# Kernel tuning notes

Measured on AMD Instinct MI355X. Metric: run time of the kernel, lower is better.

## Reference

```python
import jax, jax.numpy as jnp
import numpy as np

N = 100000      # nodes
E = 1600000     # edges
NSG2 = 20000    # subgraph2 count
NSG = 2000      # subgraph count
NG = 64         # graphs
D = 64          # hidden dim
L = 5           # conv layers


def setup_inputs() -> dict:
    key = jax.random.key(0)
    ks = jax.random.split(key, 40)
    f = lambda i, shape: (jax.random.normal(ks[i], shape, jnp.float32) * 0.05)
    inp = {
        'z': jax.random.randint(ks[0], (N, 2), 0, 100),
        'edge_index': jax.random.randint(ks[1], (2, E), 0, N),
        'node_to_subgraph2': jax.random.randint(ks[2], (N,), 0, NSG2),
        'subgraph2_to_subgraph': jax.random.randint(ks[3], (NSG2,), 0, NSG),
        'subgraph_to_graph': jax.random.randint(ks[4], (NSG,), 0, NG),
        # learned params (stacked across the 5 layers where identical shape)
        'z_emb': f(5, (L, 100, D)),
        'trans_W': f(6, (L - 1, 2 * D, D)),  # transform_before_conv, layers 1..4
        'trans_b': f(7, (L - 1, D)),
        'conv_W': f(8, (L, D, D)),           # GatedGraphConv weight (num_layers=1)
        'gru_Wih': f(9, (L, D, 3 * D)),
        'gru_bih': f(10, (L, 3 * D)),
        'gru_Whh': f(11, (L, D, 3 * D)),
        'gru_bhh': f(12, (L, 3 * D)),
        'ep_W1': f(13, (D, D)), 'ep_b1': f(14, (D,)),
        'ep_W2': f(15, (D, D)), 'ep_b2': f(16, (D,)),
        'np_W1': f(17, (D, D)), 'np_b1': f(18, (D,)),
        'np_W2': f(19, (D, D)), 'np_b2': f(20, (D,)),
        'fc1_W': f(21, (D, 32)), 'fc1_b': f(22, (32,)),
        'fc2_W': f(23, (32, 16)), 'fc2_b': f(24, (16,)),
        'fc3_W': f(25, (16, 1)), 'fc3_b': f(26, (1,)),
    }
    return inp


def _gated_conv(x, src, dst, W, Wih, bih, Whh, bhh):
    # GatedGraphConv(out=64, num_layers=1): m = aggr_add(x_j @ W), x = GRUCell(m, x)
    h = x @ W                                            # [N, D]
    m = jax.ops.segment_sum(h[src], dst, num_segments=N)  # scatter-add messages
    gi = m @ Wih + bih                                   # [N, 3D]
    gh = x @ Whh + bhh
    ir, iz, inn = jnp.split(gi, 3, axis=-1)
    hr, hz, hn = jnp.split(gh, 3, axis=-1)
    r = jax.nn.sigmoid(ir + hr)
    zg = jax.nn.sigmoid(iz + hz)
    n = jnp.tanh(inn + r * hn)
    return (1.0 - zg) * n + zg * x


def reference(z, edge_index, node_to_subgraph2, subgraph2_to_subgraph, subgraph_to_graph,
              z_emb, trans_W, trans_b, conv_W, gru_Wih, gru_bih, gru_Whh, gru_bhh,
              ep_W1, ep_b1, ep_W2, ep_b2, np_W1, np_b1, np_W2, np_b2,
              fc1_W, fc1_b, fc2_W, fc2_b, fc3_W, fc3_b):
    src, dst = edge_index[0], edge_index[1]
    x = None
    for layer in range(L):
        ze = z_emb[layer][z].sum(axis=1)  # [N,2,D] -> [N,D]
        if x is None:
            x = ze
        else:
            x = jnp.concatenate([x, ze], axis=-1) @ trans_W[layer - 1] + trans_b[layer - 1]
        x = _gated_conv(x, src, dst, conv_W[layer], gru_Wih[layer], gru_bih[layer],
                        gru_Whh[layer], gru_bhh[layer])
    # 3-level add pooling with MLPs in between
    x = jax.ops.segment_sum(x, node_to_subgraph2, num_segments=NSG2)
    x = jax.nn.relu(x @ ep_W1 + ep_b1) @ ep_W2 + ep_b2
    x = jax.ops.segment_sum(x, subgraph2_to_subgraph, num_segments=NSG)
    x = jax.nn.relu(x @ np_W1 + np_b1) @ np_W2 + np_b2
    x = jax.ops.segment_sum(x, subgraph_to_graph, num_segments=NG)
    x = jax.nn.elu(x @ fc1_W + fc1_b)
    x = jax.nn.elu(x @ fc2_W + fc2_b)
    return x @ fc3_W + fc3_b  # [NG, 1]
```

## Files before the change

### kernel.cpp

```cpp
#include <hip/hip_runtime.h>
#include <hip/hip_bf16.h>

constexpr int N    = 100000;
constexpr int E    = 1600000;
constexpr int NSG2 = 20000;
constexpr int NSG  = 2000;
constexpr int NG   = 64;
constexpr int D    = 64;
constexpr int L    = 5;

constexpr int NPB   = 32;
constexpr int NBUCK = N / NPB;
constexpr int NSTR  = 8;
constexpr int SCAP  = 128;

typedef __attribute__((ext_vector_type(8))) short short8v;
typedef __attribute__((ext_vector_type(4))) float f32x4;

__device__ __forceinline__ float sigm(float x) { return 1.0f / (1.0f + expf(-x)); }
__device__ __forceinline__ float elu(float x)  { return x > 0.0f ? x : (expf(x) - 1.0f); }

__device__ __forceinline__ unsigned short f2b(float f) {
    union { float f; unsigned u; } x; x.f = f;
    unsigned r = (x.u + 0x7FFFu + ((x.u >> 16) & 1u)) >> 16;
    return (unsigned short)r;
}
__device__ __forceinline__ float b2f(unsigned short h) {
    union { unsigned u; float f; } x; x.u = (unsigned)h << 16;
    return x.f;
}

__global__ __launch_bounds__(256) void prep_kernel(const float* __restrict__ convW,
                                                   const float* __restrict__ Wih,
                                                   float* __restrict__ WihP) {
    int idx = blockIdx.x * 256 + threadIdx.x;
    if (idx >= L * 64 * 192) return;
    int l = idx / (64 * 192);
    int rem = idx % (64 * 192);
    int i = rem / 192, j = rem % 192;
    const float* W  = convW + l * 64 * 64;
    const float* Wi = Wih  + l * 64 * 192;
    float acc = 0.0f;
    for (int t = 0; t < 64; ++t) acc = fmaf(W[i * 64 + t], Wi[t * 192 + j], acc);
    WihP[idx] = acc;
}

__global__ __launch_bounds__(256) void packg_kernel(const float* __restrict__ WihP,
                                                    const float* __restrict__ gWhh,
                                                    unsigned short* __restrict__ Wgpk) {
    int idx = blockIdx.x * 256 + threadIdx.x;
    if (idx >= L * 2 * 12 * 2 * 64) return;
    int lane = idx & 63;
    int r1 = idx >> 6;
    int t  = r1 & 1;
    int r2 = r1 >> 1;
    int nt = r2 % 12;
    int lm = r2 / 12;
    int mat = lm & 1, l = lm >> 1;
    const float* W = mat ? (gWhh + (size_t)l * 64 * 192) : (WihP + (size_t)l * 64 * 192);
    int n  = nt * 16 + (lane & 15);
    int k0 = t * 32 + (lane >> 4) * 8;
    short8v v;
#pragma unroll
    for (int j = 0; j < 8; ++j) v[j] = (short)f2b(W[(k0 + j) * 192 + n]);
    *(short8v*)(Wgpk + (size_t)idx * 8) = v;
}

__global__ __launch_bounds__(256) void packt_kernel(const float* __restrict__ tW,
                                                    unsigned short* __restrict__ tWpk) {
    int idx = blockIdx.x * 256 + threadIdx.x;
    if (idx >= (L - 1) * 4 * 4 * 64) return;
    int lane = idx & 63;
    int r1 = idx >> 6;
    int t  = r1 & 3;
    int r2 = r1 >> 2;
    int nt = r2 & 3;
    int lm = r2 >> 2;
    const float* W = tW + (size_t)lm * 128 * 64;
    int n  = nt * 16 + (lane & 15);
    int k0 = t * 32 + (lane >> 4) * 8;
    short8v v;
#pragma unroll
    for (int j = 0; j < 8; ++j) v[j] = (short)f2b(W[(k0 + j) * 64 + n]);
    *(short8v*)(tWpk + (size_t)idx * 8) = v;
}

__global__ void bucketA_kernel(const int* __restrict__ src, const int* __restrict__ dst,
                               int* __restrict__ bcnt, unsigned* __restrict__ tmp) {
    int stripe = blockIdx.x & (NSTR - 1);
    for (int e = blockIdx.x * blockDim.x + threadIdx.x; e < E; e += gridDim.x * blockDim.x) {
        int d = dst[e];
        int cell = (d >> 5) * NSTR + stripe;
        int pos = atomicAdd(&bcnt[cell * 16], 1);
        if (pos < SCAP)
            tmp[(size_t)cell * SCAP + pos] = ((unsigned)(d & 31) << 17) | (unsigned)src[e];
    }
}

__global__ __launch_bounds__(1024) void bscan_kernel(const int* __restrict__ bcnt,
                                                     int* __restrict__ bbase,
                                                     int* __restrict__ rowptrN) {
    __shared__ int part[1024];
    int t = threadIdx.x;
    int loc[4]; int sum = 0;
#pragma unroll
    for (int j = 0; j < 4; ++j) {
        int b = t * 4 + j; int v = 0;
        if (b < NBUCK) {
#pragma unroll
            for (int s = 0; s < NSTR; ++s) v += min(bcnt[(b * NSTR + s) * 16], SCAP);
        }
        loc[j] = v; sum += v;
    }
    part[t] = sum;
    __syncthreads();
    for (int off = 1; off < 1024; off <<= 1) {
        int u = (t >= off) ? part[t - off] : 0;
        __syncthreads();
        part[t] += u;
        __syncthreads();
    }
    int run = part[t] - sum;
#pragma unroll
    for (int j = 0; j < 4; ++j) {
        int b = t * 4 + j;
        if (b < NBUCK) bbase[b] = run;
        run += loc[j];
    }
    if (t == 1023) { bbase[NBUCK] = part[1023]; rowptrN[0] = part[1023]; }
}

__global__ __launch_bounds__(256) void bucketB_kernel(const unsigned* __restrict__ tmp,
                                                      const int* __restrict__ bcnt,
                                                      const int* __restrict__ bbase,
                                                      int* __restrict__ rowptr,
                                                      int* __restrict__ col) {
    __shared__ unsigned recs[NSTR * SCAP];
    __shared__ int scnt[NSTR];
    __shared__ int soff[NSTR + 1];
    __shared__ int cur[NPB];
    int b = blockIdx.x, tid = threadIdx.x;
    if (tid < NSTR) scnt[tid] = min(bcnt[(b * NSTR + tid) * 16], SCAP);
    if (tid < NPB) cur[tid] = 0;
    __syncthreads();
    if (tid == 0) {
        int r = 0;
        for (int s = 0; s < NSTR; ++s) { soff[s] = r; r += scnt[s]; }
        soff[NSTR] = r;
    }
    __syncthreads();
    int total = soff[NSTR];
    for (int i = tid; i < NSTR * SCAP; i += 256) {
        int s = i >> 7, k = i & (SCAP - 1);
        if (k < scnt[s]) recs[soff[s] + k] = tmp[((size_t)b * NSTR + s) * SCAP + k];
    }
    __syncthreads();
    for (int i = tid; i < total; i += 256) atomicAdd(&cur[recs[i] >> 17], 1);
    __syncthreads();
    if (tid == 0) {
        int base = bbase[b], r = 0;
        for (int j = 0; j < NPB; ++j) {
            int v = cur[j];
            cur[j] = base + r;
            rowptr[b * NPB + j] = base + r;
            r += v;
        }
    }
    __syncthreads();
    for (int i = tid; i < total; i += 256) {
        unsigned w = recs[i];
        int pos = atomicAdd(&cur[w >> 17], 1);
        col[pos] = (int)(w & 0x1FFFFu);
    }
}

__global__ __launch_bounds__(256) void embed_kernel(const int* __restrict__ z,
                                                    const float* __restrict__ zemb0,
                                                    float* __restrict__ x,
                                                    unsigned short* __restrict__ xb) {
    int idx = blockIdx.x * 256 + threadIdx.x;
    if (idx >= N * D) return;
    int n = idx >> 6, c = idx & 63;
    float v = zemb0[z[n * 2] * 64 + c] + zemb0[z[n * 2 + 1] * 64 + c];
    x[idx] = v;
    xb[idx] = f2b(v);
}

__global__ __launch_bounds__(256) void aggregate_kernel(const unsigned short* __restrict__ xb,
                                                        const int* __restrict__ rowptr,
                                                        const int* __restrict__ col,
                                                        unsigned short* __restrict__ sb) {
    int node = blockIdx.x * 4 + (threadIdx.x >> 6);
    int lane = threadIdx.x & 63;
    if (node >= N) return;
    int grp = lane >> 3;
    int cl  = lane & 7;
    int beg = rowptr[node], end = rowptr[node + 1];

    float a[8] = {};
    int i = beg + grp;
    for (; i + 8 < end; i += 16) {
        int u0 = col[i], u1 = col[i + 8];
        short8v v0 = *(const short8v*)(xb + (size_t)u0 * 64 + cl * 8);
        short8v v1 = *(const short8v*)(xb + (size_t)u1 * 64 + cl * 8);
#pragma unroll
        for (int j = 0; j < 8; ++j)
            a[j] += b2f((unsigned short)v0[j]) + b2f((unsigned short)v1[j]);
    }
    if (i < end) {
        int u = col[i];
        short8v v = *(const short8v*)(xb + (size_t)u * 64 + cl * 8);
#pragma unroll
        for (int j = 0; j < 8; ++j) a[j] += b2f((unsigned short)v[j]);
    }
#pragma unroll
    for (int off = 8; off < 64; off <<= 1)
#pragma unroll
        for (int j = 0; j < 8; ++j) a[j] += __shfl_xor(a[j], off, 64);
    if (grp == 0) {
        short8v r;
#pragma unroll
        for (int j = 0; j < 8; ++j) r[j] = (short)f2b(a[j]);
        *(short8v*)(sb + (size_t)node * 64 + cl * 8) = r;
    }
}

__global__ __launch_bounds__(256) void gru_mfma_kernel(const unsigned short* __restrict__ sb,
                                                       float* __restrict__ xbuf,
                                                       unsigned short* __restrict__ xb,
                                                       const unsigned short* __restrict__ Wgpk_l,
                                                       const float* __restrict__ bih,
                                                       const float* __restrict__ bhh) {
    __shared__ unsigned short s_lds[32][72];
    __shared__ unsigned short x_lds[32][72];
    int tid = threadIdx.x;
    int node0 = blockIdx.x * 32;

    {
        const float4* sb4 = (const float4*)(sb + (size_t)node0 * 64);
        const float4* xb4 = (const float4*)(xb + (size_t)node0 * 64);
        int r = tid >> 3, u = tid & 7;
        *(float4*)&s_lds[r][u * 8] = sb4[tid];
        *(float4*)&x_lds[r][u * 8] = xb4[tid];
    }
    __syncthreads();

    int lane = tid & 63, w = tid >> 6;
    int lr = lane & 15, lg = lane >> 4;

    short8v as_[2][2], ax_[2][2];
#pragma unroll
    for (int mt = 0; mt < 2; ++mt)
#pragma unroll
        for (int t = 0; t < 2; ++t) {
            int row = mt * 16 + lr, koff = t * 32 + lg * 8;
            as_[mt][t] = *(const short8v*)&s_lds[row][koff];
            ax_[mt][t] = *(const short8v*)&x_lds[row][koff];
        }

    f32x4 accA[3][2] = {};
    f32x4 accB[3][2] = {};
#pragma unroll
    for (int g = 0; g < 3; ++g) {
        int nt = g * 4 + w;
#pragma unroll
        for (int t = 0; t < 2; ++t) {
            const unsigned short* pA = Wgpk_l + ((size_t)((0 * 12 + nt) * 2 + t) * 64 + lane) * 8;
            const unsigned short* pB = Wgpk_l + ((size_t)((1 * 12 + nt) * 2 + t) * 64 + lane) * 8;
            short8v bA = *(const short8v*)pA;
            short8v bB = *(const short8v*)pB;
#pragma unroll
            for (int mt = 0; mt < 2; ++mt) {
                accA[g][mt] = __builtin_amdgcn_mfma_f32_16x16x32_bf16(as_[mt][t], bA, accA[g][mt], 0, 0, 0);
                accB[g][mt] = __builtin_amdgcn_mfma_f32_16x16x32_bf16(ax_[mt][t], bB, accB[g][mt], 0, 0, 0);
            }
        }
    }

    int ch = w * 16 + lr;
    float bi0 = bih[ch], bi1 = bih[64 + ch], bi2 = bih[128 + ch];
    float bh0 = bhh[ch], bh1 = bhh[64 + ch], bh2 = bhh[128 + ch];
#pragma unroll
    for (int mt = 0; mt < 2; ++mt) {
#pragma unroll
        for (int reg = 0; reg < 4; ++reg) {
            int m = mt * 16 + lg * 4 + reg;
            float r  = sigm(accA[0][mt][reg] + bi0 + accB[0][mt][reg] + bh0);
            float zg = sigm(accA[1][mt][reg] + bi1 + accB[1][mt][reg] + bh1);
            float nn = tanhf(accA[2][mt][reg] + bi2 + r * (accB[2][mt][reg] + bh2));
            size_t o = (size_t)(node0 + m) * 64 + ch;
            float xo = (1.0f - zg) * nn + zg * xbuf[o];
            xbuf[o] = xo;
            xb[o] = f2b(xo);
        }
    }
}

__global__ __launch_bounds__(256) void trans_mfma_kernel(const int* __restrict__ z,
                                                         const float* __restrict__ zemb_l,
                                                         const unsigned short* __restrict__ tWpk_l,
                                                         const float* __restrict__ tb,
                                                         float* __restrict__ xbuf,
                                                         unsigned short* __restrict__ xb) {
    __shared__ unsigned short a_lds[32][136];
    int tid = threadIdx.x;
    int node0 = blockIdx.x * 32;

    {
        const float4* xb4 = (const float4*)(xb + (size_t)node0 * 64);
        int r = tid >> 3, u = tid & 7;
        *(float4*)&a_lds[r][u * 8] = xb4[tid];
    }
#pragma unroll
    for (int it = 0; it < 8; ++it) {
        int idx = it * 256 + tid;
        int n = idx >> 6, k = idx & 63;
        int z0 = z[(node0 + n) * 2], z1 = z[(node0 + n) * 2 + 1];
        float ze = zemb_l[z0 * 64 + k] + zemb_l[z1 * 64 + k];
        a_lds[n][64 + k] = f2b(ze);
    }
    __syncthreads();

    int lane = tid & 63, w = tid >> 6;
    int lr = lane & 15, lg = lane >> 4;

    f32x4 acc[2] = {};
#pragma unroll
    for (int t = 0; t < 4; ++t) {
        const unsigned short* pB = tWpk_l + ((size_t)(w * 4 + t) * 64 + lane) * 8;
        short8v bf = *(const short8v*)pB;
#pragma unroll
        for (int mt = 0; mt < 2; ++mt) {
            int row = mt * 16 + lr, koff = t * 32 + lg * 8;
            short8v af = *(const short8v*)&a_lds[row][koff];
            acc[mt] = __builtin_amdgcn_mfma_f32_16x16x32_bf16(af, bf, acc[mt], 0, 0, 0);
        }
    }
    int ch = w * 16 + lr;
    float tbc = tb[ch];
#pragma unroll
    for (int mt = 0; mt < 2; ++mt)
#pragma unroll
        for (int reg = 0; reg < 4; ++reg) {
            int m = mt * 16 + lg * 4 + reg;
            size_t o = (size_t)(node0 + m) * 64 + ch;
            float v = acc[mt][reg] + tbc;
            xbuf[o] = v;
            xb[o] = f2b(v);
        }
}

__global__ void pool_kernel(const float* __restrict__ in, const int* __restrict__ idx,
                            float* __restrict__ out, int rows) {
    int i = blockIdx.x * 256 + threadIdx.x;
    if (i >= rows * 64) return;
    int r = i >> 6, c = i & 63;
    atomicAdd(out + (size_t)idx[r] * 64 + c, in[i]);
}

__global__ __launch_bounds__(256) void mlp_kernel(float* __restrict__ buf,
                                                  const float* __restrict__ W1,
                                                  const float* __restrict__ b1,
                                                  const float* __restrict__ W2,
                                                  const float* __restrict__ b2) {
    __shared__ float in_t[4][64];
    __shared__ float h_t[4][64];
    int tid = threadIdx.x;
    int c = tid & 63, r = tid >> 6;
    int row0 = blockIdx.x * 4;
    in_t[r][c] = buf[(size_t)(row0 + r) * 64 + c];
    __syncthreads();
    float acc = b1[c];
    for (int k = 0; k < 64; ++k) acc = fmaf(in_t[r][k], W1[k * 64 + c], acc);
    h_t[r][c] = fmaxf(acc, 0.0f);
    __syncthreads();
    acc = b2[c];
    for (int k = 0; k < 64; ++k) acc = fmaf(h_t[r][k], W2[k * 64 + c], acc);
    buf[(size_t)(row0 + r) * 64 + c] = acc;
}

__global__ __launch_bounds__(256) void final_kernel(const float* __restrict__ g,
                                                    const float* __restrict__ fc1W, const float* __restrict__ fc1b,
                                                    const float* __restrict__ fc2W, const float* __restrict__ fc2b,
                                                    const float* __restrict__ fc3W, const float* __restrict__ fc3b,
                                                    float* __restrict__ out) {
    __shared__ float gt[64][64];
    __shared__ float h1[64][32];
    __shared__ float h2[64][16];
    int tid = threadIdx.x;
    for (int i = tid; i < 64 * 64; i += 256) gt[i >> 6][i & 63] = g[i];
    __syncthreads();
    for (int i = tid; i < 64 * 32; i += 256) {
        int r = i >> 5, c = i & 31;
        float acc = fc1b[c];
        for (int k = 0; k < 64; ++k) acc = fmaf(gt[r][k], fc1W[k * 32 + c], acc);
        h1[r][c] = elu(acc);
    }
    __syncthreads();
    for (int i = tid; i < 64 * 16; i += 256) {
        int r = i >> 4, c = i & 15;
        float acc = fc2b[c];
        for (int k = 0; k < 32; ++k) acc = fmaf(h1[r][k], fc2W[k * 16 + c], acc);
        h2[r][c] = elu(acc);
    }
    __syncthreads();
    if (tid < 64) {
        float acc = fc3b[0];
        for (int k = 0; k < 16; ++k) acc = fmaf(h2[tid][k], fc3W[k], acc);
        out[tid] = acc;
    }
}

extern "C" void kernel_launch(void* const* d_in, const int* in_sizes, int n_in,
                              void* d_out, int out_size, void* d_ws, size_t ws_size,
                              hipStream_t stream) {
    const int*   z     = (const int*)d_in[0];
    const int*   ei    = (const int*)d_in[1];
    const int*   n2s2  = (const int*)d_in[2];
    const int*   s22s  = (const int*)d_in[3];
    const int*   s2g   = (const int*)d_in[4];
    const float* z_emb = (const float*)d_in[5];
    const float* tW    = (const float*)d_in[6];
    const float* tb    = (const float*)d_in[7];
    const float* convW = (const float*)d_in[8];
    const float* gWih  = (const float*)d_in[9];
    const float* gbih  = (const float*)d_in[10];
    const float* gWhh  = (const float*)d_in[11];
    const float* gbhh  = (const float*)d_in[12];
    const float* epW1  = (const float*)d_in[13];
    const float* epb1  = (const float*)d_in[14];
    const float* epW2  = (const float*)d_in[15];
    const float* epb2  = (const float*)d_in[16];
    const float* npW1  = (const float*)d_in[17];
    const float* npb1  = (const float*)d_in[18];
    const float* npW2  = (const float*)d_in[19];
    const float* npb2  = (const float*)d_in[20];
    const float* fc1W  = (const float*)d_in[21];
    const float* fc1b  = (const float*)d_in[22];
    const float* fc2W  = (const float*)d_in[23];
    const float* fc2b  = (const float*)d_in[24];
    const float* fc3W  = (const float*)d_in[25];
    const float* fc3b  = (const float*)d_in[26];

    const int* srcp = ei;
    const int* dstp = ei + E;

    float*          xbuf = (float*)d_ws;
    unsigned short* xb   = (unsigned short*)(xbuf + (size_t)N * D);
    unsigned short* sb   = xb + (size_t)N * D;
    float*          WihP = (float*)(sb + (size_t)N * D);
    int*            rowptr = (int*)(WihP + L * 64 * 192);
    int*            colbuf = rowptr + (N + 1);
    int*            bbase  = colbuf + E;
    uintptr_t pal = (uintptr_t)(bbase + NBUCK + 1);
    pal = (pal + 15) & ~(uintptr_t)15;
    unsigned short* Wgpk = (unsigned short*)pal;
    unsigned short* tWpk = Wgpk + (size_t)L * 2 * 12 * 2 * 64 * 8;
    unsigned* tmp  = (unsigned*)xbuf;
    int*      bcnt = (int*)(tmp + (size_t)NBUCK * NSTR * SCAP);
    float* sg2  = (float*)colbuf;
    float* sg   = sg2 + (size_t)NSG2 * D;
    float* gbuf = sg + (size_t)NSG * D;

    hipMemsetAsync(bcnt, 0, (size_t)NBUCK * NSTR * 16 * sizeof(int), stream);

    prep_kernel<<<(L * 64 * 192 + 255) / 256, 256, 0, stream>>>(convW, gWih, WihP);
    packg_kernel<<<(L * 2 * 12 * 2 * 64 + 255) / 256, 256, 0, stream>>>(WihP, gWhh, Wgpk);
    packt_kernel<<<((L - 1) * 4 * 4 * 64 + 255) / 256, 256, 0, stream>>>(tW, tWpk);

    bucketA_kernel<<<4096, 256, 0, stream>>>(srcp, dstp, bcnt, tmp);
    bscan_kernel<<<1, 1024, 0, stream>>>(bcnt, bbase, rowptr + N);
    bucketB_kernel<<<NBUCK, 256, 0, stream>>>(tmp, bcnt, bbase, rowptr, colbuf);

    embed_kernel<<<(N * D + 255) / 256, 256, 0, stream>>>(z, z_emb, xbuf, xb);

    for (int l = 0; l < L; ++l) {
        if (l > 0) {
            trans_mfma_kernel<<<N / 32, 256, 0, stream>>>(
                z, z_emb + (size_t)l * 100 * 64,
                tWpk + (size_t)(l - 1) * 4 * 4 * 64 * 8,
                tb + (size_t)(l - 1) * 64, xbuf, xb);
        }
        aggregate_kernel<<<(N + 3) / 4, 256, 0, stream>>>(xb, rowptr, colbuf, sb);
        gru_mfma_kernel<<<N / 32, 256, 0, stream>>>(
            sb, xbuf, xb,
            Wgpk + (size_t)l * 2 * 12 * 2 * 64 * 8,
            gbih + (size_t)l * 192, gbhh + (size_t)l * 192);
    }

    hipMemsetAsync(sg2, 0, (size_t)(NSG2 + NSG + NG) * D * sizeof(float), stream);
    pool_kernel<<<(N * D + 255) / 256, 256, 0, stream>>>(xbuf, n2s2, sg2, N);
    mlp_kernel<<<NSG2 / 4, 256, 0, stream>>>(sg2, epW1, epb1, epW2, epb2);
    pool_kernel<<<(NSG2 * D + 255) / 256, 256, 0, stream>>>(sg2, s22s, sg, NSG2);
    mlp_kernel<<<NSG / 4, 256, 0, stream>>>(sg, npW1, npb1, npW2, npb2);
    pool_kernel<<<(NSG * D + 255) / 256, 256, 0, stream>>>(sg, s2g, gbuf, NSG);
    final_kernel<<<1, 256, 0, stream>>>(gbuf, fc1W, fc1b, fc2W, fc2b, fc3W, fc3b, (float*)d_out);
}
```

Baseline: 570.7 us.

## Fuse aggregation, GRU update and next-layer transform into one per-layer kernel

Merges the CSR neighbor aggregation, the GRU MFMA update and the following layer's transform into a single kernel per layer. Bf16 node features are ping-ponged between two buffers so that one layer's gather reads do not race with its writes. This removes the sb round trip through global memory, the intermediate xbuf/xb writes and two launches per layer. The cost is that aggregation is now done by one 8-lane group per node with a serial edge loop, which gives less memory-level parallelism than the previous 64-lane-per-node gather, and it raises LDS use per block. The embed kernel is also vectorized to float4.

```diff
diff --git a/kernel.cpp b/kernel.cpp
--- a/kernel.cpp
+++ b/kernel.cpp
@@ -179,75 +179,66 @@
                                                     float* __restrict__ x,
                                                     unsigned short* __restrict__ xb) {
     int idx = blockIdx.x * 256 + threadIdx.x;
-    if (idx >= N * D) return;
-    int n = idx >> 6, c = idx & 63;
-    float v = zemb0[z[n * 2] * 64 + c] + zemb0[z[n * 2 + 1] * 64 + c];
-    x[idx] = v;
-    xb[idx] = f2b(v);
-}
-
-__global__ __launch_bounds__(256) void aggregate_kernel(const unsigned short* __restrict__ xb,
-                                                        const int* __restrict__ rowptr,
-                                                        const int* __restrict__ col,
-                                                        unsigned short* __restrict__ sb) {
-    int node = blockIdx.x * 4 + (threadIdx.x >> 6);
-    int lane = threadIdx.x & 63;
-    if (node >= N) return;
-    int grp = lane >> 3;
-    int cl  = lane & 7;
-    int beg = rowptr[node], end = rowptr[node + 1];
-
-    float a[8] = {};
-    int i = beg + grp;
-    for (; i + 8 < end; i += 16) {
-        int u0 = col[i], u1 = col[i + 8];
-        short8v v0 = *(const short8v*)(xb + (size_t)u0 * 64 + cl * 8);
-        short8v v1 = *(const short8v*)(xb + (size_t)u1 * 64 + cl * 8);
-#pragma unroll
-        for (int j = 0; j < 8; ++j)
-            a[j] += b2f((unsigned short)v0[j]) + b2f((unsigned short)v1[j]);
-    }
-    if (i < end) {
-        int u = col[i];
-        short8v v = *(const short8v*)(xb + (size_t)u * 64 + cl * 8);
-#pragma unroll
-        for (int j = 0; j < 8; ++j) a[j] += b2f((unsigned short)v[j]);
-    }
-#pragma unroll
-    for (int off = 8; off < 64; off <<= 1)
-#pragma unroll
-        for (int j = 0; j < 8; ++j) a[j] += __shfl_xor(a[j], off, 64);
-    if (grp == 0) {
-        short8v r;
-#pragma unroll
-        for (int j = 0; j < 8; ++j) r[j] = (short)f2b(a[j]);
-        *(short8v*)(sb + (size_t)node * 64 + cl * 8) = r;
-    }
-}
-
-__global__ __launch_bounds__(256) void gru_mfma_kernel(const unsigned short* __restrict__ sb,
-                                                       float* __restrict__ xbuf,
-                                                       unsigned short* __restrict__ xb,
-                                                       const unsigned short* __restrict__ Wgpk_l,
-                                                       const float* __restrict__ bih,
-                                                       const float* __restrict__ bhh) {
+    if (idx >= N * 16) return;
+    int n = idx >> 4, k4 = idx & 15;
+    float4 e0 = ((const float4*)(zemb0 + (size_t)z[n * 2] * 64))[k4];
+    float4 e1 = ((const float4*)(zemb0 + (size_t)z[n * 2 + 1] * 64))[k4];
+    float4 v; v.x = e0.x + e1.x; v.y = e0.y + e1.y; v.z = e0.z + e1.z; v.w = e0.w + e1.w;
+    ((float4*)x)[idx] = v;
+    ushort4 b; b.x = f2b(v.x); b.y = f2b(v.y); b.z = f2b(v.z); b.w = f2b(v.w);
+    ((ushort4*)xb)[idx] = b;
+}
+
+template<int HAS_T>
+__global__ __launch_bounds__(256) void fused_kernel(const unsigned short* __restrict__ xb_in,
+                                                    float* __restrict__ xbuf,
+                                                    unsigned short* __restrict__ xb_out,
+                                                    const int* __restrict__ rowptr,
+                                                    const int* __restrict__ col,
+                                                    const unsigned short* __restrict__ Wgpk_l,
+                                                    const float* __restrict__ bih,
+                                                    const float* __restrict__ bhh,
+                                                    const int* __restrict__ z,
+                                                    const float* __restrict__ zemb_next,
+                                                    const unsigned short* __restrict__ tWpk_next,
+                                                    const float* __restrict__ tb_next) {
     __shared__ unsigned short s_lds[32][72];
     __shared__ unsigned short x_lds[32][72];
+    __shared__ unsigned short a_lds[32][136];
     int tid = threadIdx.x;
     int node0 = blockIdx.x * 32;
+    int lane = tid & 63, w = tid >> 6;
 
     {
-        const float4* sb4 = (const float4*)(sb + (size_t)node0 * 64);
-        const float4* xb4 = (const float4*)(xb + (size_t)node0 * 64);
-        int r = tid >> 3, u = tid & 7;
-        *(float4*)&s_lds[r][u * 8] = sb4[tid];
-        *(float4*)&x_lds[r][u * 8] = xb4[tid];
-    }
-    __syncthreads();
-
-    int lane = tid & 63, w = tid >> 6;
+        int g8 = lane >> 3, cj = lane & 7;
+        int nl = w * 8 + g8;
+        int node = node0 + nl;
+        int beg = rowptr[node], end = rowptr[node + 1];
+        float a[8] = {};
+        int i = beg;
+        for (; i + 1 < end; i += 2) {
+            int u0 = col[i], u1 = col[i + 1];
+            short8v v0 = *(const short8v*)(xb_in + (size_t)u0 * 64 + cj * 8);
+            short8v v1 = *(const short8v*)(xb_in + (size_t)u1 * 64 + cj * 8);
+#pragma unroll
+            for (int j = 0; j < 8; ++j)
+                a[j] += b2f((unsigned short)v0[j]) + b2f((unsigned short)v1[j]);
+        }
+        if (i < end) {
+            int u = col[i];
+            short8v v = *(const short8v*)(xb_in + (size_t)u * 64 + cj * 8);
+#pragma unroll
+            for (int j = 0; j < 8; ++j) a[j] += b2f((unsigned short)v[j]);
+        }
+        short8v r;
+#pragma unroll
+        for (int j = 0; j < 8; ++j) r[j] = (short)f2b(a[j]);
+        *(short8v*)&s_lds[nl][cj * 8] = r;
+        *(float4*)&x_lds[nl][cj * 8] = ((const float4*)(xb_in + (size_t)node * 64))[cj];
+    }
+    __syncthreads();
+
     int lr = lane & 15, lg = lane >> 4;
-
     short8v as_[2][2], ax_[2][2];
 #pragma unroll
     for (int mt = 0; mt < 2; ++mt)
@@ -280,6 +271,7 @@
     int ch = w * 16 + lr;
     float bi0 = bih[ch], bi1 = bih[64 + ch], bi2 = bih[128 + ch];
     float bh0 = bhh[ch], bh1 = bhh[64 + ch], bh2 = bhh[128 + ch];
+    float xo[2][4];
 #pragma unroll
     for (int mt = 0; mt < 2; ++mt) {
 #pragma unroll
@@ -288,65 +280,64 @@
             float r  = sigm(accA[0][mt][reg] + bi0 + accB[0][mt][reg] + bh0);
             float zg = sigm(accA[1][mt][reg] + bi1 + accB[1][mt][reg] + bh1);
             float nn = tanhf(accA[2][mt][reg] + bi2 + r * (accB[2][mt][reg] + bh2));
-            size_t o = (size_t)(node0 + m) * 64 + ch;
-            float xo = (1.0f - zg) * nn + zg * xbuf[o];
-            xbuf[o] = xo;
-            xb[o] = f2b(xo);
-        }
-    }
-}
-
-__global__ __launch_bounds__(256) void trans_mfma_kernel(const int* __restrict__ z,
-                                                         const float* __restrict__ zemb_l,
-                                                         const unsigned short* __restrict__ tWpk_l,
-                                                         const float* __restrict__ tb,
-                                                         float* __restrict__ xbuf,
-                                                         unsigned short* __restrict__ xb) {
-    __shared__ unsigned short a_lds[32][136];
-    int tid = threadIdx.x;
-    int node0 = blockIdx.x * 32;
-
-    {
-        const float4* xb4 = (const float4*)(xb + (size_t)node0 * 64);
-        int r = tid >> 3, u = tid & 7;
-        *(float4*)&a_lds[r][u * 8] = xb4[tid];
-    }
-#pragma unroll
-    for (int it = 0; it < 8; ++it) {
+            xo[mt][reg] = (1.0f - zg) * nn + zg * xbuf[(size_t)(node0 + m) * 64 + ch];
+        }
+    }
+
+    if (HAS_T == 0) {
+#pragma unroll
+        for (int mt = 0; mt < 2; ++mt)
+#pragma unroll
+            for (int reg = 0; reg < 4; ++reg) {
+                int m = mt * 16 + lg * 4 + reg;
+                xbuf[(size_t)(node0 + m) * 64 + ch] = xo[mt][reg];
+            }
+        return;
+    }
+
+#pragma unroll
+    for (int mt = 0; mt < 2; ++mt)
+#pragma unroll
+        for (int reg = 0; reg < 4; ++reg) {
+            int m = mt * 16 + lg * 4 + reg;
+            a_lds[m][ch] = f2b(xo[mt][reg]);
+        }
+#pragma unroll
+    for (int it = 0; it < 2; ++it) {
         int idx = it * 256 + tid;
-        int n = idx >> 6, k = idx & 63;
+        int n = idx >> 4, k4 = idx & 15;
         int z0 = z[(node0 + n) * 2], z1 = z[(node0 + n) * 2 + 1];
-        float ze = zemb_l[z0 * 64 + k] + zemb_l[z1 * 64 + k];
-        a_lds[n][64 + k] = f2b(ze);
-    }
-    __syncthreads();
-
-    int lane = tid & 63, w = tid >> 6;
-    int lr = lane & 15, lg = lane >> 4;
-
-    f32x4 acc[2] = {};
+        float4 e0 = ((const float4*)(zemb_next + (size_t)z0 * 64))[k4];
+        float4 e1 = ((const float4*)(zemb_next + (size_t)z1 * 64))[k4];
+        ushort4 b;
+        b.x = f2b(e0.x + e1.x); b.y = f2b(e0.y + e1.y);
+        b.z = f2b(e0.z + e1.z); b.w = f2b(e0.w + e1.w);
+        *(ushort4*)&a_lds[n][64 + k4 * 4] = b;
+    }
+    __syncthreads();
+
+    f32x4 tacc[2] = {};
 #pragma unroll
     for (int t = 0; t < 4; ++t) {
-        const unsigned short* pB = tWpk_l + ((size_t)(w * 4 + t) * 64 + lane) * 8;
+        const unsigned short* pB = tWpk_next + ((size_t)(w * 4 + t) * 64 + lane) * 8;
         short8v bf = *(const short8v*)pB;
 #pragma unroll
         for (int mt = 0; mt < 2; ++mt) {
             int row = mt * 16 + lr, koff = t * 32 + lg * 8;
             short8v af = *(const short8v*)&a_lds[row][koff];
-            acc[mt] = __builtin_amdgcn_mfma_f32_16x16x32_bf16(af, bf, acc[mt], 0, 0, 0);
-        }
-    }
-    int ch = w * 16 + lr;
-    float tbc = tb[ch];
+            tacc[mt] = __builtin_amdgcn_mfma_f32_16x16x32_bf16(af, bf, tacc[mt], 0, 0, 0);
+        }
+    }
+    float tbc = tb_next[ch];
 #pragma unroll
     for (int mt = 0; mt < 2; ++mt)
 #pragma unroll
         for (int reg = 0; reg < 4; ++reg) {
             int m = mt * 16 + lg * 4 + reg;
             size_t o = (size_t)(node0 + m) * 64 + ch;
-            float v = acc[mt][reg] + tbc;
+            float v = tacc[mt][reg] + tbc;
             xbuf[o] = v;
-            xb[o] = f2b(v);
+            xb_out[o] = f2b(v);
         }
 }
 
@@ -446,9 +437,9 @@
     const int* dstp = ei + E;
 
     float*          xbuf = (float*)d_ws;
-    unsigned short* xb   = (unsigned short*)(xbuf + (size_t)N * D);
-    unsigned short* sb   = xb + (size_t)N * D;
-    float*          WihP = (float*)(sb + (size_t)N * D);
+    unsigned short* xbA  = (unsigned short*)(xbuf + (size_t)N * D);
+    unsigned short* xbB  = xbA + (size_t)N * D;
+    float*          WihP = (float*)(xbB + (size_t)N * D);
     int*            rowptr = (int*)(WihP + L * 64 * 192);
     int*            colbuf = rowptr + (N + 1);
     int*            bbase  = colbuf + E;
@@ -472,20 +463,25 @@
     bscan_kernel<<<1, 1024, 0, stream>>>(bcnt, bbase, rowptr + N);
     bucketB_kernel<<<NBUCK, 256, 0, stream>>>(tmp, bcnt, bbase, rowptr, colbuf);
 
-    embed_kernel<<<(N * D + 255) / 256, 256, 0, stream>>>(z, z_emb, xbuf, xb);
+    embed_kernel<<<(N * 16 + 255) / 256, 256, 0, stream>>>(z, z_emb, xbuf, xbA);
 
     for (int l = 0; l < L; ++l) {
-        if (l > 0) {
-            trans_mfma_kernel<<<N / 32, 256, 0, stream>>>(
-                z, z_emb + (size_t)l * 100 * 64,
-                tWpk + (size_t)(l - 1) * 4 * 4 * 64 * 8,
-                tb + (size_t)(l - 1) * 64, xbuf, xb);
-        }
-        aggregate_kernel<<<(N + 3) / 4, 256, 0, stream>>>(xb, rowptr, colbuf, sb);
-        gru_mfma_kernel<<<N / 32, 256, 0, stream>>>(
-            sb, xbuf, xb,
-            Wgpk + (size_t)l * 2 * 12 * 2 * 64 * 8,
-            gbih + (size_t)l * 192, gbhh + (size_t)l * 192);
+        const unsigned short* xin = (l & 1) ? xbB : xbA;
+        unsigned short*       xout = (l & 1) ? xbA : xbB;
+        if (l < L - 1) {
+            fused_kernel<1><<<N / 32, 256, 0, stream>>>(
+                xin, xbuf, xout, rowptr, colbuf,
+                Wgpk + (size_t)l * 2 * 12 * 2 * 64 * 8,
+                gbih + (size_t)l * 192, gbhh + (size_t)l * 192,
+                z, z_emb + (size_t)(l + 1) * 100 * 64,
+                tWpk + (size_t)l * 4 * 4 * 64 * 8, tb + (size_t)l * 64);
+        } else {
+            fused_kernel<0><<<N / 32, 256, 0, stream>>>(
+                xin, xbuf, nullptr, rowptr, colbuf,
+                Wgpk + (size_t)l * 2 * 12 * 2 * 64 * 8,
+                gbih + (size_t)l * 192, gbhh + (size_t)l * 192,
+                z, z_emb, tWpk, tb);
+        }
     }
 
     hipMemsetAsync(sg2, 0, (size_t)(NSG2 + NSG + NG) * D * sizeof(float), stream);
```

After: 555.1 us. -2.7%, faster.
